# Optimization experiments

Hardware: AMD Instinct MI355X
Metric: run time of the kernel (lower is better)

## Reference

```python
import jax, jax.numpy as jnp
import numpy as np

N = 8192
IN_F = 512
OUT_F = 128
ALPHA = 0.2  # leaky relu negative slope
NEG_BIG = -1e10
RND_SCALE = 1e5


def setup_inputs() -> dict:
    key = jax.random.key(0)
    k1, k2, k3, k4, k5 = jax.random.split(key, 5)
    h = jax.random.normal(k1, (N, IN_F), dtype=jnp.float32)
    adj = jax.random.randint(k2, (N, N), 0, 2, dtype=jnp.int32)
    W = jax.random.normal(k3, (IN_F, OUT_F), dtype=jnp.float32) * 0.05
    a = jax.random.normal(k4, (2 * OUT_F, 1), dtype=jnp.float32) * 0.1
    # rnd in original is 1e5*(rand-0.5); same distribution here
    rnd = RND_SCALE * (jax.random.uniform(k5, (N, OUT_F), dtype=jnp.float32) - 0.5)
    return {"h": h, "adj": adj, "W": W, "a": a, "rnd": rnd}


def reference(h, adj, W, a, rnd):
    Wh = h @ W                              # [N, OUT_F]
    Wh1 = Wh @ a[:OUT_F, :]                 # [N, 1]
    Wh2 = Wh @ a[OUT_F:, :]                 # [N, 1]
    e = jax.nn.leaky_relu(Wh1 + Wh2.T, negative_slope=ALPHA)  # [N, N]
    attention = jnp.where(adj > 0, e, NEG_BIG)
    attention = jax.nn.softmax(attention, axis=1)
    h_prime = attention @ Wh                # [N, OUT_F]
    h_prime = (h_prime + rnd) / RND_SCALE
    return jax.nn.elu(h_prime)
```

## Files before the change

### kernel.cpp

```cpp
#include <hip/hip_runtime.h>

#define N 8192
#define IN_F 512
#define OUT_F 128
#define NW (N / 8)
#define SPLITK 8
#define KC 1024
#define LOG2E 1.4426950408889634f
#define LN2 0.6931471805599453f

typedef __attribute__((ext_vector_type(4))) float f32x4;
typedef __attribute__((ext_vector_type(8))) short bf16x8;
typedef __attribute__((ext_vector_type(8))) unsigned short u16x8;
typedef __attribute__((ext_vector_type(4))) int i32x4;

__device__ __forceinline__ short f2bf(float f) {
    union { float f; unsigned u; } c; c.f = f;
    unsigned r = c.u + 0x7FFFu + ((c.u >> 16) & 1u);
    return (short)(r >> 16);
}

__device__ __forceinline__ float exp2fast(float x) {
#if __has_builtin(__builtin_amdgcn_exp2f)
    return __builtin_amdgcn_exp2f(x);
#else
    return __expf(x * LN2);
#endif
}

__device__ __forceinline__ void load_lds16(const void* g, void* l) {
    __builtin_amdgcn_global_load_lds((const __attribute__((address_space(1))) unsigned*)g,
                                     (__attribute__((address_space(3))) unsigned*)l,
                                     16, 0, 0);
}

__global__ __launch_bounds__(256) void prep(const int* __restrict__ adj,
                                            unsigned char* __restrict__ maskR,
                                            const float* __restrict__ W,
                                            short* __restrict__ WT) {
    if (blockIdx.x >= 2048) {
        int idx = (blockIdx.x - 2048) * 256 + threadIdx.x;
        int n = idx & (OUT_F - 1);
        int k = idx >> 7;
        WT[(size_t)n * IN_F + k] = f2bf(W[idx]);
        return;
    }
    const int wave = threadIdx.x >> 6, lane = threadIdx.x & 63;
    const size_t m = (size_t)blockIdx.x * 4 + wave;
    const i32x4* ap = (const i32x4*)(adj + m * N);
    unsigned char* mp = maskR + m * NW;
#pragma unroll 4
    for (int it = 0; it < 16; it++) {
        int b4 = it * 128 + lane * 2;
        i32x4 a0 = __builtin_nontemporal_load(ap + b4);
        i32x4 a1 = __builtin_nontemporal_load(ap + b4 + 1);
        unsigned b = (unsigned)(a0.x > 0) | ((unsigned)(a0.y > 0) << 1) |
                     ((unsigned)(a0.z > 0) << 2) | ((unsigned)(a0.w > 0) << 3) |
                     ((unsigned)(a1.x > 0) << 4) | ((unsigned)(a1.y > 0) << 5) |
                     ((unsigned)(a1.z > 0) << 6) | ((unsigned)(a1.w > 0) << 7);
        mp[it * 64 + lane] = (unsigned char)b;
    }
}

__global__ __launch_bounds__(256) void gemm_hW(const float* __restrict__ h,
                                               const short* __restrict__ WT,
                                               const float* __restrict__ a,
                                               short* __restrict__ WhT,
                                               float* __restrict__ sOut,
                                               float* __restrict__ tOut) {
    const int tid = threadIdx.x;
    const int wave = tid >> 6, lane = tid & 63;
    const int row16 = lane & 15, kgrp = lane >> 4;
    const int m0 = blockIdx.x * 16;
    const int kbase = wave * 128;

    f32x4 acc[8] = {};
    const float4* hp = (const float4*)(h + (size_t)(m0 + row16) * IN_F + kbase);

#pragma unroll
    for (int kk = 0; kk < 128; kk += 32) {
        float4 u0 = hp[kk / 4 + kgrp * 2];
        float4 u1 = hp[kk / 4 + kgrp * 2 + 1];
        bf16x8 af;
        af[0] = f2bf(u0.x); af[1] = f2bf(u0.y); af[2] = f2bf(u0.z); af[3] = f2bf(u0.w);
        af[4] = f2bf(u1.x); af[5] = f2bf(u1.y); af[6] = f2bf(u1.z); af[7] = f2bf(u1.w);
#pragma unroll
        for (int nt = 0; nt < 8; nt++) {
            bf16x8 bf_ = *(const bf16x8*)(WT + (size_t)(nt * 16 + row16) * IN_F + kbase + kk + kgrp * 8);
            acc[nt] = __builtin_amdgcn_mfma_f32_16x16x32_bf16(af, bf_, acc[nt], 0, 0, 0);
        }
    }

    __shared__ float red[4][16][132];
#pragma unroll
    for (int nt = 0; nt < 8; nt++)
#pragma unroll
        for (int r = 0; r < 4; r++)
            red[wave][kgrp * 4 + r][nt * 16 + row16] = acc[nt][r];
    __syncthreads();

    const int row = tid >> 4, seg = tid & 15;
    float v[8];
#pragma unroll
    for (int e = 0; e < 8; e++) {
        int c = seg * 8 + e;
        v[e] = red[0][row][c] + red[1][row][c] + red[2][row][c] + red[3][row][c];
    }
    float sp = 0.f, tp = 0.f;
#pragma unroll
    for (int e = 0; e < 8; e++) {
        sp += v[e] * a[seg * 8 + e];
        tp += v[e] * a[OUT_F + seg * 8 + e];
    }
    sp += __shfl_xor(sp, 1); tp += __shfl_xor(tp, 1);
    sp += __shfl_xor(sp, 2); tp += __shfl_xor(tp, 2);
    sp += __shfl_xor(sp, 4); tp += __shfl_xor(tp, 4);
    sp += __shfl_xor(sp, 8); tp += __shfl_xor(tp, 8);
    if (seg == 0) {
        sOut[m0 + row] = sp * LOG2E;
        tOut[m0 + row] = tp * LOG2E;
    }
#pragma unroll
    for (int e = 0; e < 8; e++)
        WhT[(size_t)(seg * 8 + e) * N + m0 + row] = f2bf(v[e]);
}

__global__ __launch_bounds__(256, 4) void attn(const unsigned char* __restrict__ maskR,
                                               const short* __restrict__ WhT,
                                               const float* __restrict__ s,
                                               const float* __restrict__ t,
                                               unsigned short* __restrict__ num,
                                               float* __restrict__ lpart) {
    const int tid = threadIdx.x;
    const int wave = tid >> 6, lane = tid & 63;
    const int row16 = lane & 15, kgrp = lane >> 4;
    const int kb = blockIdx.x & 7;
    const int mb = blockIdx.x >> 3;
    const int m0 = mb * 64 + wave * 16;
    const int m  = m0 + row16;
    const int ks = kb * KC;

    __shared__ short Bs[2][2][128 * 32];
    __shared__ float tl[KC];

    for (int i = tid; i < KC; i += 256) tl[i] = t[ks + i];

    const float s_m = s[m];
    const int4* mp = (const int4*)(maskR + (size_t)m * NW + (ks >> 3));
    int4 mcur = mp[0], mnxt = mp[1];

    auto stageB = [&](int sup, int par) {
        const int k0 = ks + sup * 64;
#pragma unroll
        for (int d = 0; d < 2; d++)
#pragma unroll
            for (int q = 0; q < 2; q++) {
                int nrow = wave * 32 + q * 16 + (lane >> 2);
                const short* g = WhT + (size_t)nrow * N + k0 + d * 32 + (lane & 3) * 8;
                load_lds16(g, &Bs[par][d][(wave * 32 + q * 16) * 32]);
            }
    };

    f32x4 acc[8] = {};
    float lsum = 0.f;

    stageB(0, 0);
    __syncthreads();

    for (int sp2 = 0; sp2 < 8; sp2++) {
#pragma unroll
        for (int ss = 0; ss < 2; ss++) {
            const int sp = sp2 * 2 + ss;
            const int par = sp & 1;
            if (sp + 1 < 16) stageB(sp + 1, par ^ 1);
#pragma unroll
            for (int d = 0; d < 2; d++) {
                const int g = sp * 2 + d;
                const unsigned dw = (unsigned)((const int*)&mcur)[ss * 2 + d];
                const unsigned mbyte = (dw >> (kgrp * 8)) & 0xFFu;

                const float* tp = tl + g * 32 + kgrp * 8;
                float4 tA = *(const float4*)tp;
                float4 tB = *(const float4*)(tp + 4);
                float tv[8] = { tA.x, tA.y, tA.z, tA.w, tB.x, tB.y, tB.z, tB.w };

                bf16x8 bfr[8];
                const short* base = &Bs[par][d][0];
#pragma unroll
                for (int ni = 0; ni < 8; ni++)
                    bfr[ni] = *(const bf16x8*)(base + (ni * 16 + row16) * 32 + kgrp * 8);

                unsigned pu[8];
#pragma unroll
                for (int e = 0; e < 8; e++) {
                    float x = s_m + tv[e];
                    x = fmaxf(x, 0.2f * x);
                    float p = exp2fast(x);
                    unsigned u = __float_as_uint(p) & 0xFFFF0000u;
                    u = ((mbyte >> e) & 1u) ? u : 0u;
                    lsum += __uint_as_float(u);
                    pu[e] = u;
                }
                bf16x8 af;
                unsigned* au = (unsigned*)&af;
#pragma unroll
                for (int q = 0; q < 4; q++) au[q] = (pu[2 * q] >> 16) | pu[2 * q + 1];
#pragma unroll
                for (int ni = 0; ni < 8; ni++)
                    acc[ni] = __builtin_amdgcn_mfma_f32_16x16x32_bf16(af, bfr[ni], acc[ni], 0, 0, 0);
            }
            __syncthreads();
        }
        mcur = mnxt;
        if (sp2 + 2 < 8) mnxt = mp[sp2 + 2];
    }

    {
        float v = lsum;
        v += __shfl_xor(v, 16);
        v += __shfl_xor(v, 32);
        if (kgrp == 0) lpart[(size_t)kb * N + m] = v;
    }

    unsigned short* np_ = num + ((size_t)kb * N + m0) * OUT_F;
#pragma unroll
    for (int ni = 0; ni < 8; ni++) {
        int n = ni * 16 + row16;
#pragma unroll
        for (int r = 0; r < 4; r++)
            np_[(size_t)(kgrp * 4 + r) * OUT_F + n] = (unsigned short)f2bf(acc[ni][r]);
    }
}

__global__ __launch_bounds__(256) void finalize(const unsigned short* __restrict__ num,
                                                const float* __restrict__ lpart,
                                                const float* __restrict__ rnd,
                                                float* __restrict__ out) {
    int idx = blockIdx.x * 256 + threadIdx.x;
    int m = idx >> 4;
    int c = (idx & 15) * 8;
    size_t g = (size_t)m * OUT_F + c;

    float nm[8] = {};
#pragma unroll
    for (int bk = 0; bk < SPLITK; bk++) {
        u16x8 v = *(const u16x8*)(num + (size_t)bk * N * OUT_F + g);
#pragma unroll
        for (int e = 0; e < 8; e++) nm[e] += __uint_as_float((unsigned)v[e] << 16);
    }
    float l = 0.f;
#pragma unroll
    for (int bk = 0; bk < SPLITK; bk++) l += lpart[(size_t)bk * N + m];
    float inv = 1.f / fmaxf(l, 1e-30f);

    float4 r0 = *(const float4*)(rnd + g);
    float4 r1 = *(const float4*)(rnd + g + 4);
    float rv[8] = { r0.x, r0.y, r0.z, r0.w, r1.x, r1.y, r1.z, r1.w };
    float ov[8];
#pragma unroll
    for (int e = 0; e < 8; e++) {
        float x = (nm[e] * inv + rv[e]) * 1e-5f;
        ov[e] = x > 0.f ? x : __expf(x) - 1.f;
    }
    *(float4*)(out + g)     = make_float4(ov[0], ov[1], ov[2], ov[3]);
    *(float4*)(out + g + 4) = make_float4(ov[4], ov[5], ov[6], ov[7]);
}

extern "C" void kernel_launch(void* const* d_in, const int* in_sizes, int n_in,
                              void* d_out, int out_size, void* d_ws, size_t ws_size,
                              hipStream_t stream) {
    const float* h   = (const float*)d_in[0];
    const int*   adj = (const int*)d_in[1];
    const float* W   = (const float*)d_in[2];
    const float* a   = (const float*)d_in[3];
    const float* rnd = (const float*)d_in[4];
    float* out = (float*)d_out;

    char* w = (char*)d_ws;
    short* WT    = (short*)(w);
    short* WhT   = (short*)(w + 131072);
    float* sv    = (float*)(w + 2228224);
    float* tv    = (float*)(w + 2260992);
    float* lpart = (float*)(w + 2293760);
    unsigned char* maskR = (unsigned char*)(w + 2555904);
    unsigned short* num  = (unsigned short*)(w + 10944512);

    prep    <<<2304, 256, 0, stream>>>(adj, maskR, W, WT);
    gemm_hW <<<512, 256, 0, stream>>>(h, WT, a, WhT, sv, tv);
    attn    <<<1024, 256, 0, stream>>>(maskR, WhT, sv, tv, num, lpart);
    finalize<<<(N * OUT_F / 8) / 256, 256, 0, stream>>>(num, lpart, rnd, out);
}
```

Before: 408.6 us.

## Fuse adjacency bitmask packing into attention kernel with register prefetch

Removes the separate prep pass that packed the int32 adjacency into a bitmask, and instead has the attention kernel stream adj rows directly with nontemporal loads, double-buffered in registers two super-steps ahead. The syncthreads is replaced by explicit waitcnt plus barrier so that the outstanding adj prefetch loads need not drain before each barrier. This drops one full write and re-read of the mask plus a kernel launch, at the cost of more registers in attn and mask compares inside the hot loop.

```diff
diff --git a/kernel.cpp b/kernel.cpp
--- a/kernel.cpp
+++ b/kernel.cpp
@@ -3,7 +3,6 @@
 #define N 8192
 #define IN_F 512
 #define OUT_F 128
-#define NW (N / 8)
 #define SPLITK 8
 #define KC 1024
 #define LOG2E 1.4426950408889634f
@@ -34,32 +33,11 @@
                                      16, 0, 0);
 }
 
-__global__ __launch_bounds__(256) void prep(const int* __restrict__ adj,
-                                            unsigned char* __restrict__ maskR,
-                                            const float* __restrict__ W,
-                                            short* __restrict__ WT) {
-    if (blockIdx.x >= 2048) {
-        int idx = (blockIdx.x - 2048) * 256 + threadIdx.x;
-        int n = idx & (OUT_F - 1);
-        int k = idx >> 7;
-        WT[(size_t)n * IN_F + k] = f2bf(W[idx]);
-        return;
-    }
-    const int wave = threadIdx.x >> 6, lane = threadIdx.x & 63;
-    const size_t m = (size_t)blockIdx.x * 4 + wave;
-    const i32x4* ap = (const i32x4*)(adj + m * N);
-    unsigned char* mp = maskR + m * NW;
-#pragma unroll 4
-    for (int it = 0; it < 16; it++) {
-        int b4 = it * 128 + lane * 2;
-        i32x4 a0 = __builtin_nontemporal_load(ap + b4);
-        i32x4 a1 = __builtin_nontemporal_load(ap + b4 + 1);
-        unsigned b = (unsigned)(a0.x > 0) | ((unsigned)(a0.y > 0) << 1) |
-                     ((unsigned)(a0.z > 0) << 2) | ((unsigned)(a0.w > 0) << 3) |
-                     ((unsigned)(a1.x > 0) << 4) | ((unsigned)(a1.y > 0) << 5) |
-                     ((unsigned)(a1.z > 0) << 6) | ((unsigned)(a1.w > 0) << 7);
-        mp[it * 64 + lane] = (unsigned char)b;
-    }
+__global__ __launch_bounds__(256) void conv_W(const float* __restrict__ W, short* __restrict__ WT) {
+    int idx = blockIdx.x * 256 + threadIdx.x;
+    int n = idx & (OUT_F - 1);
+    int k = idx >> 7;
+    WT[(size_t)n * IN_F + k] = f2bf(W[idx]);
 }
 
 __global__ __launch_bounds__(256) void gemm_hW(const float* __restrict__ h,
@@ -125,7 +103,7 @@
         WhT[(size_t)(seg * 8 + e) * N + m0 + row] = f2bf(v[e]);
 }
 
-__global__ __launch_bounds__(256, 4) void attn(const unsigned char* __restrict__ maskR,
+__global__ __launch_bounds__(256, 4) void attn(const int* __restrict__ adj,
                                                const short* __restrict__ WhT,
                                                const float* __restrict__ s,
                                                const float* __restrict__ t,
@@ -146,8 +124,7 @@
     for (int i = tid; i < KC; i += 256) tl[i] = t[ks + i];
 
     const float s_m = s[m];
-    const int4* mp = (const int4*)(maskR + (size_t)m * NW + (ks >> 3));
-    int4 mcur = mp[0], mnxt = mp[1];
+    const i32x4* arow = (const i32x4*)(adj + (size_t)m * N + ks + kgrp * 8);
 
     auto stageB = [&](int sup, int par) {
         const int k0 = ks + sup * 64;
@@ -161,59 +138,80 @@
             }
     };
 
+    i32x4 G[2][4];
+#pragma unroll
+    for (int p = 0; p < 2; p++)
+#pragma unroll
+        for (int j = 0; j < 4; j++)
+            G[p][j] = __builtin_nontemporal_load(arow + p * 16 + (j >> 1) * 8 + (j & 1));
+
     f32x4 acc[8] = {};
     float lsum = 0.f;
 
     stageB(0, 0);
     __syncthreads();
 
-    for (int sp2 = 0; sp2 < 8; sp2++) {
-#pragma unroll
-        for (int ss = 0; ss < 2; ss++) {
-            const int sp = sp2 * 2 + ss;
-            const int par = sp & 1;
-            if (sp + 1 < 16) stageB(sp + 1, par ^ 1);
-#pragma unroll
-            for (int d = 0; d < 2; d++) {
-                const int g = sp * 2 + d;
-                const unsigned dw = (unsigned)((const int*)&mcur)[ss * 2 + d];
-                const unsigned mbyte = (dw >> (kgrp * 8)) & 0xFFu;
-
-                const float* tp = tl + g * 32 + kgrp * 8;
-                float4 tA = *(const float4*)tp;
-                float4 tB = *(const float4*)(tp + 4);
-                float tv[8] = { tA.x, tA.y, tA.z, tA.w, tB.x, tB.y, tB.z, tB.w };
-
-                bf16x8 bfr[8];
-                const short* base = &Bs[par][d][0];
-#pragma unroll
-                for (int ni = 0; ni < 8; ni++)
-                    bfr[ni] = *(const bf16x8*)(base + (ni * 16 + row16) * 32 + kgrp * 8);
-
-                unsigned pu[8];
-#pragma unroll
-                for (int e = 0; e < 8; e++) {
-                    float x = s_m + tv[e];
-                    x = fmaxf(x, 0.2f * x);
-                    float p = exp2fast(x);
-                    unsigned u = __float_as_uint(p) & 0xFFFF0000u;
-                    u = ((mbyte >> e) & 1u) ? u : 0u;
-                    lsum += __uint_as_float(u);
-                    pu[e] = u;
-                }
-                bf16x8 af;
-                unsigned* au = (unsigned*)&af;
-#pragma unroll
-                for (int q = 0; q < 4; q++) au[q] = (pu[2 * q] >> 16) | pu[2 * q + 1];
-#pragma unroll
-                for (int ni = 0; ni < 8; ni++)
-                    acc[ni] = __builtin_amdgcn_mfma_f32_16x16x32_bf16(af, bfr[ni], acc[ni], 0, 0, 0);
+    auto super_body = [&](int sp, bool dostage, bool doadj) {
+        const int par = sp & 1;
+        if (dostage) stageB(sp + 1, par ^ 1);
+        unsigned mbyte[2];
+#pragma unroll
+        for (int d = 0; d < 2; d++) {
+            i32x4 a0 = G[par][d * 2], a1 = G[par][d * 2 + 1];
+            mbyte[d] = (a0.x > 0 ? 1u : 0u) | (a0.y > 0 ? 2u : 0u) |
+                       (a0.z > 0 ? 4u : 0u) | (a0.w > 0 ? 8u : 0u) |
+                       (a1.x > 0 ? 16u : 0u) | (a1.y > 0 ? 32u : 0u) |
+                       (a1.z > 0 ? 64u : 0u) | (a1.w > 0 ? 128u : 0u);
+        }
+        if (doadj) {
+#pragma unroll
+            for (int j = 0; j < 4; j++)
+                G[par][j] = __builtin_nontemporal_load(arow + (sp + 2) * 16 + (j >> 1) * 8 + (j & 1));
+        }
+#pragma unroll
+        for (int d = 0; d < 2; d++) {
+            const int g = sp * 2 + d;
+            const float* tp = tl + g * 32 + kgrp * 8;
+            float4 tA = *(const float4*)tp;
+            float4 tB = *(const float4*)(tp + 4);
+            float tv[8] = { tA.x, tA.y, tA.z, tA.w, tB.x, tB.y, tB.z, tB.w };
+
+            bf16x8 bfr[8];
+            const short* base = &Bs[par][d][0];
+#pragma unroll
+            for (int ni = 0; ni < 8; ni++)
+                bfr[ni] = *(const bf16x8*)(base + (ni * 16 + row16) * 32 + kgrp * 8);
+
+            unsigned pu[8];
+#pragma unroll
+            for (int e = 0; e < 8; e++) {
+                float x = s_m + tv[e];
+                x = fmaxf(x, 0.2f * x);
+                float p = exp2fast(x);
+                unsigned u = __float_as_uint(p) & 0xFFFF0000u;
+                u = ((mbyte[d] >> e) & 1u) ? u : 0u;
+                lsum += __uint_as_float(u);
+                pu[e] = u;
             }
-            __syncthreads();
-        }
-        mcur = mnxt;
-        if (sp2 + 2 < 8) mnxt = mp[sp2 + 2];
-    }
+            bf16x8 af;
+            unsigned* au = (unsigned*)&af;
+#pragma unroll
+            for (int q = 0; q < 4; q++) au[q] = (pu[2 * q] >> 16) | pu[2 * q + 1];
+#pragma unroll
+            for (int ni = 0; ni < 8; ni++)
+                acc[ni] = __builtin_amdgcn_mfma_f32_16x16x32_bf16(af, bfr[ni], acc[ni], 0, 0, 0);
+        }
+    };
+
+    for (int sp = 0; sp < 14; sp++) {
+        super_body(sp, true, true);
+        __builtin_amdgcn_s_waitcnt(0x0F74);
+        __builtin_amdgcn_s_barrier();
+    }
+    super_body(14, true, false);
+    __builtin_amdgcn_s_waitcnt(0x0F70);
+    __builtin_amdgcn_s_barrier();
+    super_body(15, false, false);
 
     {
         float v = lsum;
@@ -282,11 +280,10 @@
     float* sv    = (float*)(w + 2228224);
     float* tv    = (float*)(w + 2260992);
     float* lpart = (float*)(w + 2293760);
-    unsigned char* maskR = (unsigned char*)(w + 2555904);
-    unsigned short* num  = (unsigned short*)(w + 10944512);
-
-    prep    <<<2304, 256, 0, stream>>>(adj, maskR, W, WT);
+    unsigned short* num = (unsigned short*)(w + 2555904);
+
+    conv_W  <<<256, 256, 0, stream>>>(W, WT);
     gemm_hW <<<512, 256, 0, stream>>>(h, WT, a, WhT, sv, tv);
-    attn    <<<1024, 256, 0, stream>>>(maskR, WhT, sv, tv, num, lpart);
+    attn    <<<1024, 256, 0, stream>>>(adj, WhT, sv, tv, num, lpart);
     finalize<<<(N * OUT_F / 8) / 256, 256, 0, stream>>>(num, lpart, rnd, out);
 }
```

Measured after the change: 415.7 us. No clear change (+1.7%).

## Give each attention wave two 16-row M tiles to reuse staged B fragments

Applied to the files above, without the earlier changes.

Each wave in the attention kernel now handles 32 rows as two 16-row MFMA tiles instead of one. The WhT B fragments loaded from LDS are reused across both tiles, and the grid is halved to 512 blocks. This cuts LDS traffic and staging work per output row, but doubles the accumulator registers, so the occupancy hint drops from 4 to 3. The mask prep kernel also switches from nontemporal loads to plain loads.

```diff
diff --git a/kernel.cpp b/kernel.cpp
--- a/kernel.cpp
+++ b/kernel.cpp
@@ -52,8 +52,7 @@
 #pragma unroll 4
     for (int it = 0; it < 16; it++) {
         int b4 = it * 128 + lane * 2;
-        i32x4 a0 = __builtin_nontemporal_load(ap + b4);
-        i32x4 a1 = __builtin_nontemporal_load(ap + b4 + 1);
+        i32x4 a0 = ap[b4], a1 = ap[b4 + 1];
         unsigned b = (unsigned)(a0.x > 0) | ((unsigned)(a0.y > 0) << 1) |
                      ((unsigned)(a0.z > 0) << 2) | ((unsigned)(a0.w > 0) << 3) |
                      ((unsigned)(a1.x > 0) << 4) | ((unsigned)(a1.y > 0) << 5) |
@@ -125,7 +124,7 @@
         WhT[(size_t)(seg * 8 + e) * N + m0 + row] = f2bf(v[e]);
 }
 
-__global__ __launch_bounds__(256, 4) void attn(const unsigned char* __restrict__ maskR,
+__global__ __launch_bounds__(256, 3) void attn(const unsigned char* __restrict__ maskR,
                                                const short* __restrict__ WhT,
                                                const float* __restrict__ s,
                                                const float* __restrict__ t,
@@ -136,8 +135,7 @@
     const int row16 = lane & 15, kgrp = lane >> 4;
     const int kb = blockIdx.x & 7;
     const int mb = blockIdx.x >> 3;
-    const int m0 = mb * 64 + wave * 16;
-    const int m  = m0 + row16;
+    const int m0w = mb * 128 + wave * 32;
     const int ks = kb * KC;
 
     __shared__ short Bs[2][2][128 * 32];
@@ -145,9 +143,17 @@
 
     for (int i = tid; i < KC; i += 256) tl[i] = t[ks + i];
 
-    const float s_m = s[m];
-    const int4* mp = (const int4*)(maskR + (size_t)m * NW + (ks >> 3));
-    int4 mcur = mp[0], mnxt = mp[1];
+    float s_m[2];
+    const int4* mp[2];
+#pragma unroll
+    for (int mi = 0; mi < 2; mi++) {
+        int m = m0w + mi * 16 + row16;
+        s_m[mi] = s[m];
+        mp[mi] = (const int4*)(maskR + (size_t)m * NW + (ks >> 3));
+    }
+    int4 mcur[2], mnxt[2];
+#pragma unroll
+    for (int mi = 0; mi < 2; mi++) { mcur[mi] = mp[mi][0]; mnxt[mi] = mp[mi][1]; }
 
     auto stageB = [&](int sup, int par) {
         const int k0 = ks + sup * 64;
@@ -161,8 +167,8 @@
             }
     };
 
-    f32x4 acc[8] = {};
-    float lsum = 0.f;
+    f32x4 acc[2][8] = {};
+    float lsum[2] = {0.f, 0.f};
 
     stageB(0, 0);
     __syncthreads();
@@ -176,9 +182,6 @@
 #pragma unroll
             for (int d = 0; d < 2; d++) {
                 const int g = sp * 2 + d;
-                const unsigned dw = (unsigned)((const int*)&mcur)[ss * 2 + d];
-                const unsigned mbyte = (dw >> (kgrp * 8)) & 0xFFu;
-
                 const float* tp = tl + g * 32 + kgrp * 8;
                 float4 tA = *(const float4*)tp;
                 float4 tB = *(const float4*)(tp + 4);
@@ -190,45 +193,56 @@
                 for (int ni = 0; ni < 8; ni++)
                     bfr[ni] = *(const bf16x8*)(base + (ni * 16 + row16) * 32 + kgrp * 8);
 
-                unsigned pu[8];
-#pragma unroll
-                for (int e = 0; e < 8; e++) {
-                    float x = s_m + tv[e];
-                    x = fmaxf(x, 0.2f * x);
-                    float p = exp2fast(x);
-                    unsigned u = __float_as_uint(p) & 0xFFFF0000u;
-                    u = ((mbyte >> e) & 1u) ? u : 0u;
-                    lsum += __uint_as_float(u);
-                    pu[e] = u;
+#pragma unroll
+                for (int mi = 0; mi < 2; mi++) {
+                    const unsigned dw = (unsigned)((const int*)&mcur[mi])[ss * 2 + d];
+                    const unsigned mbyte = (dw >> (kgrp * 8)) & 0xFFu;
+                    unsigned pu[8];
+#pragma unroll
+                    for (int e = 0; e < 8; e++) {
+                        float x = s_m[mi] + tv[e];
+                        x = fmaxf(x, 0.2f * x);
+                        float p = exp2fast(x);
+                        unsigned u = __float_as_uint(p) & 0xFFFF0000u;
+                        u = ((mbyte >> e) & 1u) ? u : 0u;
+                        lsum[mi] += __uint_as_float(u);
+                        pu[e] = u;
+                    }
+                    bf16x8 af;
+                    unsigned* au = (unsigned*)&af;
+#pragma unroll
+                    for (int q = 0; q < 4; q++) au[q] = (pu[2 * q] >> 16) | pu[2 * q + 1];
+#pragma unroll
+                    for (int ni = 0; ni < 8; ni++)
+                        acc[mi][ni] = __builtin_amdgcn_mfma_f32_16x16x32_bf16(af, bfr[ni], acc[mi][ni], 0, 0, 0);
                 }
-                bf16x8 af;
-                unsigned* au = (unsigned*)&af;
-#pragma unroll
-                for (int q = 0; q < 4; q++) au[q] = (pu[2 * q] >> 16) | pu[2 * q + 1];
-#pragma unroll
-                for (int ni = 0; ni < 8; ni++)
-                    acc[ni] = __builtin_amdgcn_mfma_f32_16x16x32_bf16(af, bfr[ni], acc[ni], 0, 0, 0);
             }
             __syncthreads();
         }
-        mcur = mnxt;
-        if (sp2 + 2 < 8) mnxt = mp[sp2 + 2];
-    }
-
-    {
-        float v = lsum;
+#pragma unroll
+        for (int mi = 0; mi < 2; mi++) {
+            mcur[mi] = mnxt[mi];
+            if (sp2 + 2 < 8) mnxt[mi] = mp[mi][sp2 + 2];
+        }
+    }
+
+#pragma unroll
+    for (int mi = 0; mi < 2; mi++) {
+        float v = lsum[mi];
         v += __shfl_xor(v, 16);
         v += __shfl_xor(v, 32);
-        if (kgrp == 0) lpart[(size_t)kb * N + m] = v;
-    }
-
-    unsigned short* np_ = num + ((size_t)kb * N + m0) * OUT_F;
-#pragma unroll
-    for (int ni = 0; ni < 8; ni++) {
-        int n = ni * 16 + row16;
-#pragma unroll
-        for (int r = 0; r < 4; r++)
-            np_[(size_t)(kgrp * 4 + r) * OUT_F + n] = (unsigned short)f2bf(acc[ni][r]);
+        if (kgrp == 0) lpart[(size_t)kb * N + m0w + mi * 16 + row16] = v;
+    }
+    unsigned short* np_ = num + ((size_t)kb * N + m0w) * OUT_F;
+#pragma unroll
+    for (int mi = 0; mi < 2; mi++) {
+#pragma unroll
+        for (int ni = 0; ni < 8; ni++) {
+            int n = ni * 16 + row16;
+#pragma unroll
+            for (int r = 0; r < 4; r++)
+                np_[(size_t)(mi * 16 + kgrp * 4 + r) * OUT_F + n] = (unsigned short)f2bf(acc[mi][ni][r]);
+        }
     }
 }
 
@@ -287,6 +301,6 @@
 
     prep    <<<2304, 256, 0, stream>>>(adj, maskR, W, WT);
     gemm_hW <<<512, 256, 0, stream>>>(h, WT, a, WhT, sv, tv);
-    attn    <<<1024, 256, 0, stream>>>(maskR, WhT, sv, tv, num, lpart);
+    attn    <<<512, 256, 0, stream>>>(maskR, WhT, sv, tv, num, lpart);
     finalize<<<(N * OUT_F / 8) / 256, 256, 0, stream>>>(num, lpart, rnd, out);
 }
```

Measured after the change: 448.3 us. 9.7% more time.
